# Kernel tuning notes

Measured on AMD Instinct MI355X. Metric: run time of the kernel, lower is better.

## Reference

```python
import jax, jax.numpy as jnp
import numpy as np

B, T, C, H = 2, 2048, 1024, 16
HS = C // H  # 64
EPS = 1e-5


def layernorm(x, g, b):
    mu = jnp.mean(x, axis=-1, keepdims=True)
    var = jnp.var(x, axis=-1, keepdims=True)
    return (x - mu) * jax.lax.rsqrt(var + EPS) * g + b


def setup_inputs() -> dict:
    key = jax.random.key(0)
    ks = jax.random.split(key, 12)
    s = lambda fan_in: 1.0 / np.sqrt(fan_in)
    inp = {
        'x':  jax.random.normal(ks[0], (B, T, C), dtype=jnp.float32),
        'Wq': jax.random.uniform(ks[1], (H, C, HS), jnp.float32, -s(C), s(C)),
        'Wk': jax.random.uniform(ks[2], (H, C, HS), jnp.float32, -s(C), s(C)),
        'Wv': jax.random.uniform(ks[3], (H, C, HS), jnp.float32, -s(C), s(C)),
        'Wp': jax.random.uniform(ks[4], (C, C), jnp.float32, -s(C), s(C)),
        'bp': jax.random.uniform(ks[5], (C,), jnp.float32, -s(C), s(C)),
        'W1': jax.random.uniform(ks[6], (C, 4 * C), jnp.float32, -s(C), s(C)),
        'b1': jax.random.uniform(ks[7], (4 * C,), jnp.float32, -s(C), s(C)),
        'W2': jax.random.uniform(ks[8], (4 * C, C), jnp.float32, -s(4 * C), s(4 * C)),
        'b2': jax.random.uniform(ks[9], (C,), jnp.float32, -s(4 * C), s(4 * C)),
        'g1': jnp.ones((C,), jnp.float32),
        'be1': jnp.zeros((C,), jnp.float32),
        'g2': jnp.ones((C,), jnp.float32),
        'be2': jnp.zeros((C,), jnp.float32),
    }
    return inp


def block(x, Wq, Wk, Wv, Wp, bp, W1, b1, W2, b2, g1, be1, g2, be2):
    # quirky residual structure: residual is taken from the post-LN tensor
    x = layernorm(x, g1, be1)
    # batched multi-head attention (all heads at once): [B,H,T,HS]
    q = jnp.einsum('btc,hcd->bhtd', x, Wq)
    k = jnp.einsum('btc,hcd->bhtd', x, Wk)
    v = jnp.einsum('btc,hcd->bhtd', x, Wv)
    # NOTE: original scales by full embedding dim C ** -0.5, not head_size
    scores = jnp.einsum('bhtd,bhsd->bhts', q, k) * (C ** -0.5)
    causal = jnp.tril(jnp.ones((T, T), dtype=bool))
    scores = jnp.where(causal, scores, -jnp.inf)
    wei = jax.nn.softmax(scores, axis=-1)  # dropout p=0 in eval
    out = jnp.einsum('bhts,bhsd->bhtd', wei, v)
    out = out.transpose(0, 2, 1, 3).reshape(B, T, C)  # concat heads
    out = out @ Wp + bp
    x = x + out
    x = layernorm(x, g2, be2)
    ff = jax.nn.relu(x @ W1 + b1) @ W2 + b2
    return x + ff


def reference(x, Wq, Wk, Wv, Wp, bp, W1, b1, W2, b2, g1, be1, g2, be2):
    return block(x, Wq, Wk, Wv, Wp, bp, W1, b1, W2, b2, g1, be1, g2, be2)
```

## Files before the change

kernel.cpp:

```cpp
#include <hip/hip_runtime.h>
#include <hip/hip_bf16.h>
#include <cstdint>
#include <cstddef>

typedef __attribute__((ext_vector_type(8))) short short8;
typedef __attribute__((ext_vector_type(4))) float f32x4;
typedef __attribute__((ext_vector_type(16))) float f32x16;
typedef unsigned int u32;
typedef unsigned short u16;

__device__ inline u16 f2b(float x) {
    union { float f; u32 u; } v; v.f = x;
    u32 u = v.u;
    u32 r = (u + 0x7fff + ((u >> 16) & 1)) >> 16;
    return (u16)r;
}
__device__ inline float b2f(u16 h) {
    union { u32 u; float f; } v; v.u = ((u32)h) << 16;
    return v.f;
}
__device__ inline u32 cvtpk(float lo, float hi) {
    u32 r; asm("v_cvt_pk_bf16_f32 %0, %1, %2" : "=v"(r) : "v"(lo), "v"(hi)); return r;
}
__device__ inline void gll16(const void* g, void* l) {
    __builtin_amdgcn_global_load_lds(
        (const __attribute__((address_space(1))) void*)g,
        (__attribute__((address_space(3))) void*)l, 16, 0, 0);
}

__global__ __launch_bounds__(256) void repack_qkv_tiled(
    const float* __restrict__ Wq, const float* __restrict__ Wk, const float* __restrict__ Wv,
    u16* __restrict__ out)
{
    __shared__ u16 lds[64 * 72];
    const int tid = threadIdx.x;
    const int c0 = blockIdx.x * 64;
    const int sh = blockIdx.y;
    const int sel = sh >> 4, h = sh & 15;
    const float* W = (sel == 0) ? Wq : (sel == 1) ? Wk : Wv;
    #pragma unroll
    for (int it = 0; it < 4; ++it) {
        int idx = tid + it * 256;
        int c = idx >> 4, d4 = idx & 15;
        float4 v = *reinterpret_cast<const float4*>(&W[((size_t)(h * 1024 + c0 + c)) * 64 + d4 * 4]);
        lds[(d4 * 4 + 0) * 72 + c] = f2b(v.x);
        lds[(d4 * 4 + 1) * 72 + c] = f2b(v.y);
        lds[(d4 * 4 + 2) * 72 + c] = f2b(v.z);
        lds[(d4 * 4 + 3) * 72 + c] = f2b(v.w);
    }
    __syncthreads();
    #pragma unroll
    for (int it = 0; it < 2; ++it) {
        int idx = tid + it * 256;
        int d = idx >> 3, c8 = idx & 7;
        short8 s = *reinterpret_cast<const short8*>(&lds[d * 72 + c8 * 8]);
        *reinterpret_cast<short8*>(&out[((size_t)(sel * 1024 + h * 64 + d)) * 1024 + c0 + c8 * 8]) = s;
    }
}

__global__ __launch_bounds__(256) void trans_tiled(
    const float* __restrict__ in, u16* __restrict__ out, int P, int Q)
{
    __shared__ u16 lds[64 * 72];
    const int tid = threadIdx.x;
    const int p0 = blockIdx.x * 64, q0 = blockIdx.y * 64;
    #pragma unroll
    for (int it = 0; it < 4; ++it) {
        int idx = tid + it * 256;
        int p = idx >> 4, q4 = idx & 15;
        float4 v = *reinterpret_cast<const float4*>(&in[(size_t)(p0 + p) * Q + q0 + q4 * 4]);
        lds[(q4 * 4 + 0) * 72 + p] = f2b(v.x);
        lds[(q4 * 4 + 1) * 72 + p] = f2b(v.y);
        lds[(q4 * 4 + 2) * 72 + p] = f2b(v.z);
        lds[(q4 * 4 + 3) * 72 + p] = f2b(v.w);
    }
    __syncthreads();
    #pragma unroll
    for (int it = 0; it < 2; ++it) {
        int idx = tid + it * 256;
        int q = idx >> 3, p8 = idx & 7;
        short8 s = *reinterpret_cast<const short8*>(&lds[q * 72 + p8 * 8]);
        *reinterpret_cast<short8*>(&out[(size_t)(q0 + q) * P + p0 + p8 * 8]) = s;
    }
}

__global__ __launch_bounds__(256) void vt_kernel(
    const u16* __restrict__ qkv, u16* __restrict__ vt)
{
    __shared__ u16 lds[64 * 72];
    const int tid = threadIdx.x;
    const int s0 = blockIdx.x * 64, h = blockIdx.y, b = blockIdx.z;
    #pragma unroll
    for (int it = 0; it < 2; ++it) {
        int idx = tid + it * 256;
        int s = idx >> 3, d8 = idx & 7;
        short8 kv = *reinterpret_cast<const short8*>(
            &qkv[((size_t)(b * 2048 + s0 + s)) * 3072 + 2048 + h * 64 + d8 * 8]);
        #pragma unroll
        for (int j = 0; j < 8; ++j) lds[(d8 * 8 + j) * 72 + s] = (u16)kv[j];
    }
    __syncthreads();
    #pragma unroll
    for (int it = 0; it < 2; ++it) {
        int idx = tid + it * 256;
        int d = idx >> 3, s8 = idx & 7;
        short8 s = *reinterpret_cast<const short8*>(&lds[d * 72 + s8 * 8]);
        *reinterpret_cast<short8*>(&vt[((size_t)(b * 16 + h) * 64 + d) * 2048 + s0 + s8 * 8]) = s;
    }
}

__global__ __launch_bounds__(256) void ln_kernel(
    const float* __restrict__ x, const float* __restrict__ g, const float* __restrict__ be,
    float* __restrict__ yf, u16* __restrict__ yb)
{
    int row = blockIdx.x;
    const float4 v = reinterpret_cast<const float4*>(x + (size_t)row * 1024)[threadIdx.x];
    float s  = v.x + v.y + v.z + v.w;
    float s2 = v.x * v.x + v.y * v.y + v.z * v.z + v.w * v.w;
    #pragma unroll
    for (int o = 32; o >= 1; o >>= 1) { s += __shfl_xor(s, o); s2 += __shfl_xor(s2, o); }
    __shared__ float red[8];
    int w = threadIdx.x >> 6;
    if ((threadIdx.x & 63) == 0) { red[w] = s; red[4 + w] = s2; }
    __syncthreads();
    s  = red[0] + red[1] + red[2] + red[3];
    s2 = red[4] + red[5] + red[6] + red[7];
    float mu = s * (1.0f / 1024.0f);
    float var = s2 * (1.0f / 1024.0f) - mu * mu;
    float rs = rsqrtf(var + 1e-5f);
    const float4 gg = reinterpret_cast<const float4*>(g)[threadIdx.x];
    const float4 bb = reinterpret_cast<const float4*>(be)[threadIdx.x];
    float4 o;
    o.x = (v.x - mu) * rs * gg.x + bb.x;
    o.y = (v.y - mu) * rs * gg.y + bb.y;
    o.z = (v.z - mu) * rs * gg.z + bb.z;
    o.w = (v.w - mu) * rs * gg.w + bb.w;
    reinterpret_cast<float4*>(yf + (size_t)row * 1024)[threadIdx.x] = o;
    uint2 pk;
    pk.x = (u32)f2b(o.x) | ((u32)f2b(o.y) << 16);
    pk.y = (u32)f2b(o.z) | ((u32)f2b(o.w) << 16);
    reinterpret_cast<uint2*>(yb + (size_t)row * 1024)[threadIdx.x] = pk;
}

template<bool BIAS, bool RELU, bool RESID, bool OUTB>
__global__ __launch_bounds__(256) void gemm_bt(
    const u16* __restrict__ A, int lda,
    const u16* __restrict__ BT, int ldb,
    void* __restrict__ out, int ldo,
    const float* __restrict__ bias,
    const float* __restrict__ resid,
    int K)
{
    __shared__ __align__(16) char smem[64 * 1024];
    const int tid = threadIdx.x;
    const int lane = tid & 63, w = tid >> 6;
    const int wr = w >> 1, wc = w & 1;
    const int l15 = lane & 15, lq = lane >> 4;

    const int nx = gridDim.x;
    const int nwg = nx * gridDim.y;
    int orig = blockIdx.y * nx + blockIdx.x;
    int wgid = orig;
    if ((nwg & 7) == 0) wgid = (orig & 7) * (nwg >> 3) + (orig >> 3);
    const int m0 = (wgid / nx) * 128, n0 = (wgid % nx) * 128;

    auto stage = [&](int kt, int buf) {
        char* As = smem + buf * 32768;
        char* Bs = smem + buf * 32768 + 16384;
        #pragma unroll
        for (int it = 0; it < 4; ++it) {
            int slot = it * 256 + tid;
            int row = slot >> 3, c8 = (slot & 7) ^ (row & 7);
            gll16(A + (size_t)(m0 + row) * lda + kt + c8 * 8, As + (it * 256 + w * 64) * 16);
        }
        #pragma unroll
        for (int it = 0; it < 4; ++it) {
            int slot = it * 256 + tid;
            int row = slot >> 3, c8 = (slot & 7) ^ (row & 7);
            gll16(BT + (size_t)(n0 + row) * ldb + kt + c8 * 8, Bs + (it * 256 + w * 64) * 16);
        }
    };

    f32x4 acc[4][4] = {};
    const int nk = K >> 6;

    stage(0, 0);
    __syncthreads();

    for (int t = 0; t < nk; ++t) {
        const char* As = smem + (t & 1) * 32768;
        const char* Bs = smem + (t & 1) * 32768 + 16384;
        if (t + 1 < nk) stage((t + 1) << 6, (t + 1) & 1);
        #pragma unroll
        for (int kk = 0; kk < 2; ++kk) {
            const int sc = kk * 4 + lq;
            short8 a[4], b[4];
            #pragma unroll
            for (int mi = 0; mi < 4; ++mi) {
                int row = wr * 64 + mi * 16 + l15;
                a[mi] = *reinterpret_cast<const short8*>(As + row * 128 + ((sc ^ (row & 7)) << 4));
            }
            #pragma unroll
            for (int ni = 0; ni < 4; ++ni) {
                int row = wc * 64 + ni * 16 + l15;
                b[ni] = *reinterpret_cast<const short8*>(Bs + row * 128 + ((sc ^ (row & 7)) << 4));
            }
            #pragma unroll
            for (int mi = 0; mi < 4; ++mi)
                #pragma unroll
                for (int ni = 0; ni < 4; ++ni)
                    acc[mi][ni] = __builtin_amdgcn_mfma_f32_16x16x32_bf16(a[mi], b[ni], acc[mi][ni], 0, 0, 0);
        }
        __syncthreads();
    }

    #pragma unroll
    for (int mi = 0; mi < 4; ++mi) {
        #pragma unroll
        for (int ni = 0; ni < 4; ++ni) {
            int col = n0 + wc * 64 + ni * 16 + l15;
            float bv = BIAS ? bias[col] : 0.0f;
            #pragma unroll
            for (int r = 0; r < 4; ++r) {
                int row = m0 + wr * 64 + mi * 16 + lq * 4 + r;
                float v = acc[mi][ni][r] + bv;
                if (RELU) v = v > 0.0f ? v : 0.0f;
                if (RESID) v += resid[(size_t)row * ldo + col];
                if (OUTB) ((u16*)out)[(size_t)row * ldo + col] = f2b(v);
                else      ((float*)out)[(size_t)row * ldo + col] = v;
            }
        }
    }
}

__global__ __launch_bounds__(256, 2) void attn_kernel(
    const u16* __restrict__ qkv, const u16* __restrict__ vt, u16* __restrict__ att)
{
    __shared__ __align__(16) char smem[48 * 1024];
    char* Kb0 = smem;
    char* Kb1 = smem + 8192;
    char* Vb0 = smem + 16384;
    char* Vb1 = smem + 24576;
    char* Ost = smem + 32768;

    const int tid = threadIdx.x, lane = tid & 63, w = tid >> 6;
    const int l31 = lane & 31, hi = lane >> 5;
    const int bh = blockIdx.x;
    const int qbi = 15 - blockIdx.y;
    const int b = bh >> 4, h = bh & 15;
    const size_t base = (size_t)b * 2048;
    const int q0w = qbi * 128 + w * 32;
    const int nst = 2 * qbi + 2;
    const int kcol = 1024 + h * 64;
    const u16* vtp = vt + (size_t)bh * 64 * 2048;

    const float SC = 0.03125f * 1.44269504f;

    short8 qf[4];
    {
        const u16* qp = qkv + (base + q0w + l31) * 3072 + h * 64 + hi * 8;
        #pragma unroll
        for (int dc = 0; dc < 4; ++dc) {
            short8 q = *reinterpret_cast<const short8*>(qp + dc * 16);
            #pragma unroll
            for (int j = 0; j < 8; j += 2) {
                u32 pk = cvtpk(b2f((u16)q[j]) * SC, b2f((u16)q[j + 1]) * SC);
                q[j]     = (short)(pk & 0xffff);
                q[j + 1] = (short)(pk >> 16);
            }
            qf[dc] = q;
        }
    }

    auto stage = [&](int st, char* kb, char* vb) {
        #pragma unroll
        for (int i = 0; i < 2; ++i) {
            int seg = w * 2 + i;
            int slot = seg * 64 + lane;
            int s = slot >> 3, d8p = slot & 7;
            gll16(qkv + (base + st * 64 + s) * 3072 + kcol + ((d8p ^ (s & 7)) * 8),
                  kb + seg * 1024);
            int d = s, s8p = d8p;
            gll16(vtp + (size_t)d * 2048 + st * 64 + ((s8p ^ (d & 7)) * 8),
                  vb + seg * 1024);
        }
    };

    f32x16 oT[2] = {};
    float m = -1e30f, lsum = 0.0f;
    const int qg = q0w + l31;

    stage(0, Kb0, Vb0);
    __syncthreads();

    for (int st = 0; st < nst; ++st) {
        char* kb = (st & 1) ? Kb1 : Kb0;
        char* vb = (st & 1) ? Vb1 : Vb0;
        if (st + 1 < nst) stage(st + 1, (st & 1) ? Kb0 : Kb1, (st & 1) ? Vb0 : Vb1);

        f32x16 sa[2] = {};
        #pragma unroll
        for (int dc = 0; dc < 4; ++dc) {
            #pragma unroll
            for (int sb = 0; sb < 2; ++sb) {
                int s = sb * 32 + l31;
                int slot = (dc * 2 + hi) ^ (s & 7);
                short8 kf = *reinterpret_cast<const short8*>(kb + s * 128 + slot * 16);
                sa[sb] = __builtin_amdgcn_mfma_f32_32x32x16_bf16(kf, qf[dc], sa[sb], 0, 0, 0);
            }
        }

        const bool maskt = (st >= nst - 2);
        float mx = -1e30f;
        #pragma unroll
        for (int sb = 0; sb < 2; ++sb)
            #pragma unroll
            for (int r = 0; r < 16; ++r) {
                float v = sa[sb][r];
                int sg = st * 64 + sb * 32 + (r & 3) + 8 * (r >> 2) + 4 * hi;
                if (maskt && sg > qg) v = -1e30f;
                sa[sb][r] = v;
                mx = fmaxf(mx, v);
            }
        mx = fmaxf(mx, __shfl_xor(mx, 32));
        if (!__all(mx <= m + 8.0f)) {
            float nm = fmaxf(m, mx);
            float sf = exp2f(m - nm);
            m = nm;
            lsum *= sf;
            #pragma unroll
            for (int dt = 0; dt < 2; ++dt)
                #pragma unroll
                for (int r = 0; r < 16; ++r) oT[dt][r] *= sf;
        }
        float ps = 0.0f;
        #pragma unroll
        for (int sb = 0; sb < 2; ++sb)
            #pragma unroll
            for (int r = 0; r < 16; ++r) {
                float p = exp2f(sa[sb][r] - m);
                sa[sb][r] = p;
                ps += p;
            }
        ps += __shfl_xor(ps, 32);
        lsum += ps;

        u32 pkE[4][2], pkO[4][2];
        #pragma unroll
        for (int sc = 0; sc < 4; ++sc) {
            const int sb = sc >> 1, rb = 8 * (sc & 1);
            #pragma unroll
            for (int c = 0; c < 2; ++c) {
                pkE[sc][c] = cvtpk(sa[sb][rb + 2 * c], sa[sb][rb + 2 * c + 1]);
                pkO[sc][c] = cvtpk(sa[sb][rb + 4 + 2 * c], sa[sb][rb + 4 + 2 * c + 1]);
            }
        }

        #pragma unroll
        for (int sc = 0; sc < 4; ++sc) {
            u32 wd[4];
            #pragma unroll
            for (int ww = 0; ww < 4; ++ww) {
                const int c = ww & 1;
                u32 own  = hi ? pkO[sc][c] : pkE[sc][c];
                u32 send = hi ? pkE[sc][c] : pkO[sc][c];
                u32 ex = (u32)__shfl_xor((int)send, 32);
                wd[ww] = ((ww >> 1) == hi) ? own : ex;
            }
            union { u32 u[4]; short8 s8; } pb_;
            pb_.u[0] = wd[0]; pb_.u[1] = wd[1]; pb_.u[2] = wd[2]; pb_.u[3] = wd[3];
            #pragma unroll
            for (int dt = 0; dt < 2; ++dt) {
                int d = dt * 32 + l31;
                int slot = (sc * 2 + hi) ^ (d & 7);
                short8 vf = *reinterpret_cast<const short8*>(vb + d * 128 + slot * 16);
                oT[dt] = __builtin_amdgcn_mfma_f32_32x32x16_bf16(vf, pb_.s8, oT[dt], 0, 0, 0);
            }
        }
        __syncthreads();
    }

    {
        float inv = 1.0f / lsum;
        char* ob = Ost + w * 4096;
        #pragma unroll
        for (int dt = 0; dt < 2; ++dt)
            #pragma unroll
            for (int rp = 0; rp < 8; ++rp) {
                int r = rp * 2;
                int d = dt * 32 + (r & 3) + 8 * (r >> 2) + 4 * hi;
                u32 pk2 = cvtpk(oT[dt][r] * inv, oT[dt][r + 1] * inv);
                int byte = l31 * 128 + ((((d >> 3) ^ (l31 & 7)) << 4)) + (d & 7) * 2;
                *reinterpret_cast<u32*>(ob + byte) = pk2;
            }
        __syncthreads();
        int q = lane >> 1, half = lane & 1;
        size_t grow = (base + q0w + q) * 1024 + h * 64 + half * 32;
        #pragma unroll
        for (int c = 0; c < 4; ++c) {
            int chunk = half * 4 + c;
            int byte = q * 128 + ((chunk ^ (q & 7)) << 4);
            float4 vv = *reinterpret_cast<const float4*>(ob + byte);
            *reinterpret_cast<float4*>(att + grow + c * 8) = vv;
        }
    }
}

extern "C" void kernel_launch(void* const* d_in, const int* in_sizes, int n_in,
                              void* d_out, int out_size, void* d_ws, size_t ws_size,
                              hipStream_t stream)
{
    const float* x   = (const float*)d_in[0];
    const float* Wq  = (const float*)d_in[1];
    const float* Wk  = (const float*)d_in[2];
    const float* Wv  = (const float*)d_in[3];
    const float* Wp  = (const float*)d_in[4];
    const float* bp  = (const float*)d_in[5];
    const float* W1  = (const float*)d_in[6];
    const float* b1  = (const float*)d_in[7];
    const float* W2  = (const float*)d_in[8];
    const float* b2  = (const float*)d_in[9];
    const float* g1  = (const float*)d_in[10];
    const float* be1 = (const float*)d_in[11];
    const float* g2  = (const float*)d_in[12];
    const float* be2 = (const float*)d_in[13];
    float* out = (float*)d_out;

    char* ws = (char*)d_ws;
    u16*   wqkvT = (u16*)(ws + 0);
    u16*   wpT   = (u16*)(ws + 6291456);
    u16*   w1T   = (u16*)(ws + 8388608);
    u16*   w2T   = (u16*)(ws + 16777216);
    float* xlnF  = (float*)(ws + 25165824);
    u16*   xlnB  = (u16*)(ws + 41943040);
    u16*   qkv   = (u16*)(ws + 50331648);
    float* x2    = (float*)(ws + 50331648);
    u16*   hbuf  = (u16*)(ws + 50331648);
    u16*   attb  = (u16*)(ws + 75497472);
    float* yF    = (float*)(ws + 83886080);
    u16*   vtb   = (u16*)(ws + 83886080);
    u16*   yB    = xlnB;

    repack_qkv_tiled<<<dim3(16, 48), 256, 0, stream>>>(Wq, Wk, Wv, wqkvT);
    trans_tiled<<<dim3(16, 16), 256, 0, stream>>>(Wp, wpT, 1024, 1024);
    trans_tiled<<<dim3(16, 64), 256, 0, stream>>>(W1, w1T, 1024, 4096);
    trans_tiled<<<dim3(64, 16), 256, 0, stream>>>(W2, w2T, 4096, 1024);

    ln_kernel<<<4096, 256, 0, stream>>>(x, g1, be1, xlnF, xlnB);

    gemm_bt<false, false, false, true><<<dim3(24, 32), 256, 0, stream>>>(
        xlnB, 1024, wqkvT, 1024, qkv, 3072, nullptr, nullptr, 1024);

    vt_kernel<<<dim3(32, 16, 2), 256, 0, stream>>>(qkv, vtb);
    attn_kernel<<<dim3(32, 16), 256, 0, stream>>>(qkv, vtb, attb);

    gemm_bt<true, false, true, false><<<dim3(8, 32), 256, 0, stream>>>(
        attb, 1024, wpT, 1024, x2, 1024, bp, xlnF, 1024);

    ln_kernel<<<4096, 256, 0, stream>>>(x2, g2, be2, yF, yB);

    gemm_bt<true, true, false, true><<<dim3(32, 32), 256, 0, stream>>>(
        yB, 1024, w1T, 1024, hbuf, 4096, b1, nullptr, 1024);

    gemm_bt<true, false, true, false><<<dim3(8, 32), 256, 0, stream>>>(
        hbuf, 4096, w2T, 4096, out, 1024, b2, yF, 4096);
}
```

Before: 251.4 us.

## Pair causal query blocks per workgroup and use raw v_exp with tree reductions

Each attention workgroup now handles two query blocks (qbi = 15-y and y), which balances causal work across workgroups and halves the grid. The softmax max and sum reductions become tree-shaped to shorten dependency chains, and exp2f is replaced by the raw v_exp_f32 instruction. The grid of 256 workgroups may underfill the GPU's compute units. The __syncthreads between the LDS output staging and its readback is removed; each wave reads only its own staging region, so this relies on wave-local ordering.

Result: faster. 235.8 us (-6.2%).

```diff
diff --git a/kernel.cpp b/kernel.cpp
--- a/kernel.cpp
+++ b/kernel.cpp
@@ -21,6 +21,9 @@
 }
 __device__ inline u32 cvtpk(float lo, float hi) {
     u32 r; asm("v_cvt_pk_bf16_f32 %0, %1, %2" : "=v"(r) : "v"(lo), "v"(hi)); return r;
+}
+__device__ inline float ex2(float x) {
+    float r; asm("v_exp_f32 %0, %1" : "=v"(r) : "v"(x)); return r;
 }
 __device__ inline void gll16(const void* g, void* l) {
     __builtin_amdgcn_global_load_lds(
@@ -246,31 +249,11 @@
     const int tid = threadIdx.x, lane = tid & 63, w = tid >> 6;
     const int l31 = lane & 31, hi = lane >> 5;
     const int bh = blockIdx.x;
-    const int qbi = 15 - blockIdx.y;
     const int b = bh >> 4, h = bh & 15;
     const size_t base = (size_t)b * 2048;
-    const int q0w = qbi * 128 + w * 32;
-    const int nst = 2 * qbi + 2;
     const int kcol = 1024 + h * 64;
     const u16* vtp = vt + (size_t)bh * 64 * 2048;
-
     const float SC = 0.03125f * 1.44269504f;
-
-    short8 qf[4];
-    {
-        const u16* qp = qkv + (base + q0w + l31) * 3072 + h * 64 + hi * 8;
-        #pragma unroll
-        for (int dc = 0; dc < 4; ++dc) {
-            short8 q = *reinterpret_cast<const short8*>(qp + dc * 16);
-            #pragma unroll
-            for (int j = 0; j < 8; j += 2) {
-                u32 pk = cvtpk(b2f((u16)q[j]) * SC, b2f((u16)q[j + 1]) * SC);
-                q[j]     = (short)(pk & 0xffff);
-                q[j + 1] = (short)(pk >> 16);
-            }
-            qf[dc] = q;
-        }
-    }
 
     auto stage = [&](int st, char* kb, char* vb) {
         #pragma unroll
@@ -286,122 +269,152 @@
         }
     };
 
-    f32x16 oT[2] = {};
-    float m = -1e30f, lsum = 0.0f;
-    const int qg = q0w + l31;
-
-    stage(0, Kb0, Vb0);
-    __syncthreads();
-
-    for (int st = 0; st < nst; ++st) {
-        char* kb = (st & 1) ? Kb1 : Kb0;
-        char* vb = (st & 1) ? Vb1 : Vb0;
-        if (st + 1 < nst) stage(st + 1, (st & 1) ? Kb0 : Kb1, (st & 1) ? Vb0 : Vb1);
-
-        f32x16 sa[2] = {};
-        #pragma unroll
-        for (int dc = 0; dc < 4; ++dc) {
-            #pragma unroll
-            for (int sb = 0; sb < 2; ++sb) {
-                int s = sb * 32 + l31;
-                int slot = (dc * 2 + hi) ^ (s & 7);
-                short8 kf = *reinterpret_cast<const short8*>(kb + s * 128 + slot * 16);
-                sa[sb] = __builtin_amdgcn_mfma_f32_32x32x16_bf16(kf, qf[dc], sa[sb], 0, 0, 0);
-            }
-        }
-
-        const bool maskt = (st >= nst - 2);
-        float mx = -1e30f;
-        #pragma unroll
-        for (int sb = 0; sb < 2; ++sb)
-            #pragma unroll
-            for (int r = 0; r < 16; ++r) {
-                float v = sa[sb][r];
-                int sg = st * 64 + sb * 32 + (r & 3) + 8 * (r >> 2) + 4 * hi;
-                if (maskt && sg > qg) v = -1e30f;
-                sa[sb][r] = v;
-                mx = fmaxf(mx, v);
-            }
-        mx = fmaxf(mx, __shfl_xor(mx, 32));
-        if (!__all(mx <= m + 8.0f)) {
-            float nm = fmaxf(m, mx);
-            float sf = exp2f(m - nm);
-            m = nm;
-            lsum *= sf;
+    for (int pass = 0; pass < 2; ++pass) {
+        const int qbi = pass ? (int)blockIdx.y : 15 - (int)blockIdx.y;
+        const int q0w = qbi * 128 + w * 32;
+        const int nst = 2 * qbi + 2;
+        const int qg = q0w + l31;
+
+        short8 qf[4];
+        {
+            const u16* qp = qkv + (base + q0w + l31) * 3072 + h * 64 + hi * 8;
+            #pragma unroll
+            for (int dc = 0; dc < 4; ++dc) {
+                short8 q = *reinterpret_cast<const short8*>(qp + dc * 16);
+                #pragma unroll
+                for (int j = 0; j < 8; j += 2) {
+                    u32 pk = cvtpk(b2f((u16)q[j]) * SC, b2f((u16)q[j + 1]) * SC);
+                    q[j]     = (short)(pk & 0xffff);
+                    q[j + 1] = (short)(pk >> 16);
+                }
+                qf[dc] = q;
+            }
+        }
+
+        f32x16 oT[2] = {};
+        float m = -1e30f, lsum = 0.0f;
+
+        stage(0, Kb0, Vb0);
+        __syncthreads();
+
+        for (int st = 0; st < nst; ++st) {
+            char* kb = (st & 1) ? Kb1 : Kb0;
+            char* vb = (st & 1) ? Vb1 : Vb0;
+            if (st + 1 < nst) stage(st + 1, (st & 1) ? Kb0 : Kb1, (st & 1) ? Vb0 : Vb1);
+
+            f32x16 sa[2] = {};
+            #pragma unroll
+            for (int dc = 0; dc < 4; ++dc) {
+                #pragma unroll
+                for (int sb = 0; sb < 2; ++sb) {
+                    int s = sb * 32 + l31;
+                    int slot = (dc * 2 + hi) ^ (s & 7);
+                    short8 kf = *reinterpret_cast<const short8*>(kb + s * 128 + slot * 16);
+                    sa[sb] = __builtin_amdgcn_mfma_f32_32x32x16_bf16(kf, qf[dc], sa[sb], 0, 0, 0);
+                }
+            }
+
+            if (st >= nst - 2) {
+                #pragma unroll
+                for (int sb = 0; sb < 2; ++sb)
+                    #pragma unroll
+                    for (int r = 0; r < 16; ++r) {
+                        int sg = st * 64 + sb * 32 + (r & 3) + 8 * (r >> 2) + 4 * hi;
+                        if (sg > qg) sa[sb][r] = -1e30f;
+                    }
+            }
+
+            float t8[8];
+            #pragma unroll
+            for (int i = 0; i < 8; ++i)
+                t8[i] = fmaxf(fmaxf(sa[0][i], sa[0][i + 8]), fmaxf(sa[1][i], sa[1][i + 8]));
+            float t4a = fmaxf(t8[0], t8[4]), t4b = fmaxf(t8[1], t8[5]);
+            float t4c = fmaxf(t8[2], t8[6]), t4d = fmaxf(t8[3], t8[7]);
+            float mx = fmaxf(fmaxf(t4a, t4b), fmaxf(t4c, t4d));
+            mx = fmaxf(mx, __shfl_xor(mx, 32));
+
+            if (!__all(mx <= m + 8.0f)) {
+                float nm = fmaxf(m, mx);
+                float sf = ex2(m - nm);
+                m = nm;
+                lsum *= sf;
+                #pragma unroll
+                for (int dt = 0; dt < 2; ++dt)
+                    #pragma unroll
+                    for (int r = 0; r < 16; ++r) oT[dt][r] *= sf;
+            }
+
+            #pragma unroll
+            for (int sb = 0; sb < 2; ++sb)
+                #pragma unroll
+                for (int r = 0; r < 16; ++r) sa[sb][r] = ex2(sa[sb][r] - m);
+            float s8_[8];
+            #pragma unroll
+            for (int i = 0; i < 8; ++i)
+                s8_[i] = (sa[0][i] + sa[0][i + 8]) + (sa[1][i] + sa[1][i + 8]);
+            float s4a = s8_[0] + s8_[4], s4b = s8_[1] + s8_[5];
+            float s4c = s8_[2] + s8_[6], s4d = s8_[3] + s8_[7];
+            float ps = (s4a + s4b) + (s4c + s4d);
+            ps += __shfl_xor(ps, 32);
+            lsum += ps;
+
+            u32 pkE[4][2], pkO[4][2];
+            #pragma unroll
+            for (int sc = 0; sc < 4; ++sc) {
+                const int sb = sc >> 1, rb = 8 * (sc & 1);
+                #pragma unroll
+                for (int c = 0; c < 2; ++c) {
+                    pkE[sc][c] = cvtpk(sa[sb][rb + 2 * c], sa[sb][rb + 2 * c + 1]);
+                    pkO[sc][c] = cvtpk(sa[sb][rb + 4 + 2 * c], sa[sb][rb + 4 + 2 * c + 1]);
+                }
+            }
+
+            #pragma unroll
+            for (int sc = 0; sc < 4; ++sc) {
+                u32 wd[4];
+                #pragma unroll
+                for (int ww = 0; ww < 4; ++ww) {
+                    const int c = ww & 1;
+                    u32 own  = hi ? pkO[sc][c] : pkE[sc][c];
+                    u32 send = hi ? pkE[sc][c] : pkO[sc][c];
+                    u32 ex = (u32)__shfl_xor((int)send, 32);
+                    wd[ww] = ((ww >> 1) == hi) ? own : ex;
+                }
+                union { u32 u[4]; short8 s8; } pb_;
+                pb_.u[0] = wd[0]; pb_.u[1] = wd[1]; pb_.u[2] = wd[2]; pb_.u[3] = wd[3];
+                #pragma unroll
+                for (int dt = 0; dt < 2; ++dt) {
+                    int d = dt * 32 + l31;
+                    int slot = (sc * 2 + hi) ^ (d & 7);
+                    short8 vf = *reinterpret_cast<const short8*>(vb + d * 128 + slot * 16);
+                    oT[dt] = __builtin_amdgcn_mfma_f32_32x32x16_bf16(vf, pb_.s8, oT[dt], 0, 0, 0);
+                }
+            }
+            __syncthreads();
+        }
+
+        {
+            float inv = 1.0f / lsum;
+            char* ob = Ost + w * 4096;
             #pragma unroll
             for (int dt = 0; dt < 2; ++dt)
                 #pragma unroll
-                for (int r = 0; r < 16; ++r) oT[dt][r] *= sf;
-        }
-        float ps = 0.0f;
-        #pragma unroll
-        for (int sb = 0; sb < 2; ++sb)
-            #pragma unroll
-            for (int r = 0; r < 16; ++r) {
-                float p = exp2f(sa[sb][r] - m);
-                sa[sb][r] = p;
-                ps += p;
-            }
-        ps += __shfl_xor(ps, 32);
-        lsum += ps;
-
-        u32 pkE[4][2], pkO[4][2];
-        #pragma unroll
-        for (int sc = 0; sc < 4; ++sc) {
-            const int sb = sc >> 1, rb = 8 * (sc & 1);
-            #pragma unroll
-            for (int c = 0; c < 2; ++c) {
-                pkE[sc][c] = cvtpk(sa[sb][rb + 2 * c], sa[sb][rb + 2 * c + 1]);
-                pkO[sc][c] = cvtpk(sa[sb][rb + 4 + 2 * c], sa[sb][rb + 4 + 2 * c + 1]);
-            }
-        }
-
-        #pragma unroll
-        for (int sc = 0; sc < 4; ++sc) {
-            u32 wd[4];
-            #pragma unroll
-            for (int ww = 0; ww < 4; ++ww) {
-                const int c = ww & 1;
-                u32 own  = hi ? pkO[sc][c] : pkE[sc][c];
-                u32 send = hi ? pkE[sc][c] : pkO[sc][c];
-                u32 ex = (u32)__shfl_xor((int)send, 32);
-                wd[ww] = ((ww >> 1) == hi) ? own : ex;
-            }
-            union { u32 u[4]; short8 s8; } pb_;
-            pb_.u[0] = wd[0]; pb_.u[1] = wd[1]; pb_.u[2] = wd[2]; pb_.u[3] = wd[3];
-            #pragma unroll
-            for (int dt = 0; dt < 2; ++dt) {
-                int d = dt * 32 + l31;
-                int slot = (sc * 2 + hi) ^ (d & 7);
-                short8 vf = *reinterpret_cast<const short8*>(vb + d * 128 + slot * 16);
-                oT[dt] = __builtin_amdgcn_mfma_f32_32x32x16_bf16(vf, pb_.s8, oT[dt], 0, 0, 0);
-            }
-        }
-        __syncthreads();
-    }
-
-    {
-        float inv = 1.0f / lsum;
-        char* ob = Ost + w * 4096;
-        #pragma unroll
-        for (int dt = 0; dt < 2; ++dt)
-            #pragma unroll
-            for (int rp = 0; rp < 8; ++rp) {
-                int r = rp * 2;
-                int d = dt * 32 + (r & 3) + 8 * (r >> 2) + 4 * hi;
-                u32 pk2 = cvtpk(oT[dt][r] * inv, oT[dt][r + 1] * inv);
-                int byte = l31 * 128 + ((((d >> 3) ^ (l31 & 7)) << 4)) + (d & 7) * 2;
-                *reinterpret_cast<u32*>(ob + byte) = pk2;
-            }
-        __syncthreads();
-        int q = lane >> 1, half = lane & 1;
-        size_t grow = (base + q0w + q) * 1024 + h * 64 + half * 32;
-        #pragma unroll
-        for (int c = 0; c < 4; ++c) {
-            int chunk = half * 4 + c;
-            int byte = q * 128 + ((chunk ^ (q & 7)) << 4);
-            float4 vv = *reinterpret_cast<const float4*>(ob + byte);
-            *reinterpret_cast<float4*>(att + grow + c * 8) = vv;
+                for (int rp = 0; rp < 8; ++rp) {
+                    int r = rp * 2;
+                    int d = dt * 32 + (r & 3) + 8 * (r >> 2) + 4 * hi;
+                    u32 pk2 = cvtpk(oT[dt][r] * inv, oT[dt][r + 1] * inv);
+                    int byte = l31 * 128 + ((((d >> 3) ^ (l31 & 7)) << 4)) + (d & 7) * 2;
+                    *reinterpret_cast<u32*>(ob + byte) = pk2;
+                }
+            int q = lane >> 1, half = lane & 1;
+            size_t grow = (base + q0w - w * 32 + (w * 32 + q)) * 1024 + h * 64 + half * 32;
+            #pragma unroll
+            for (int c = 0; c < 4; ++c) {
+                int chunk = half * 4 + c;
+                int byte = q * 128 + ((chunk ^ (q & 7)) << 4);
+                float4 vv = *reinterpret_cast<const float4*>(ob + byte);
+                *reinterpret_cast<float4*>(att + grow + c * 8) = vv;
+            }
         }
     }
 }
@@ -452,7 +465,7 @@
         xlnB, 1024, wqkvT, 1024, qkv, 3072, nullptr, nullptr, 1024);
 
     vt_kernel<<<dim3(32, 16, 2), 256, 0, stream>>>(qkv, vtb);
-    attn_kernel<<<dim3(32, 16), 256, 0, stream>>>(qkv, vtb, attb);
+    attn_kernel<<<dim3(32, 8), 256, 0, stream>>>(qkv, vtb, attb);
 
     gemm_bt<true, false, true, false><<<dim3(8, 32), 256, 0, stream>>>(
         attb, 1024, wpT, 1024, x2, 1024, bp, xlnF, 1024);
```
